# Optimization experiments

Measured on AMD Instinct MI355X. Metric: run time of the kernel, lower is better.

The kernel has to match this reference:

```python
import jax, jax.numpy as jnp
import numpy as np

D = 256; NH = 8; HD = D // NH; L = 4; P = 4; NQ = 900; BS = 8; DFFN = 1024
SHAPES = np.array([[128, 128], [64, 64], [32, 32], [16, 16]])  # (H, W) per level, static metadata
NV = int((SHAPES[:, 0] * SHAPES[:, 1]).sum())
EPS = 1e-6


def setup_inputs():
    key = jax.random.key(0)
    ks = iter(jax.random.split(key, 48))

    def nrm(shape, scale=0.02):
        return jax.random.normal(next(ks), shape, jnp.float32) * scale

    lsi = np.concatenate([[0], np.cumsum(SHAPES[:, 0] * SHAPES[:, 1])[:-1]]).astype(np.int64)
    return {
        'tgt': nrm((NQ, BS, D), 1.0),
        'tgt_query_pos': nrm((NQ, BS, D), 1.0),
        'tgt_reference_points': jax.random.uniform(next(ks), (NQ, BS, L, 2), jnp.float32),
        'memory': nrm((NV, BS, D), 1.0),
        'memory_spatial_shapes': jnp.asarray(SHAPES, jnp.int32),
        'memory_level_start_index': jnp.asarray(lsi, jnp.int32),
        'w_norm_sa': jnp.ones((D,), jnp.float32),
        'w_norm_ca': jnp.ones((D,), jnp.float32),
        'w_norm_ffn': jnp.ones((D,), jnp.float32),
        'ls_sa': jnp.full((D,), 1e-4, jnp.float32),
        'ls_ca': jnp.full((D,), 1e-4, jnp.float32),
        'ls_ffn': jnp.full((D,), 1e-4, jnp.float32),
        'Wq': nrm((D, D)), 'Wk': nrm((D, D)), 'Wv': nrm((D, D)),
        'bq': jnp.zeros((D,), jnp.float32), 'bk': jnp.zeros((D,), jnp.float32), 'bv': jnp.zeros((D,), jnp.float32),
        'Wo_sa': nrm((D, D)), 'bo_sa': jnp.zeros((D,), jnp.float32),
        'Wv_proj': nrm((D, D)), 'bv_proj': jnp.zeros((D,), jnp.float32),
        'W_off': nrm((NH * L * P * 2, D)), 'b_off': nrm((NH * L * P * 2,), 0.1),
        'W_attn': nrm((NH * L * P, D)), 'b_attn': jnp.zeros((NH * L * P,), jnp.float32),
        'W_out_ca': nrm((D, D)), 'bo_ca': jnp.zeros((D,), jnp.float32),
        'Wg': nrm((DFFN, D)), 'bg': jnp.zeros((DFFN,), jnp.float32),
        'Wu': nrm((DFFN, D)), 'bu': jnp.zeros((DFFN,), jnp.float32),
        'Wf': nrm((D, DFFN)), 'bf': jnp.zeros((D,), jnp.float32),
    }


def rmsnorm(x, w):
    return x * jax.lax.rsqrt(jnp.mean(x * x, axis=-1, keepdims=True) + EPS) * w


def ms_deform_sample(v, loc, attw):
    # v: (bs, nv, NH, HD); loc: (bs, nq, NH, L, P, 2) normalized (x, y); attw: (bs, nq, NH, L, P)
    bs, nq = loc.shape[0], loc.shape[1]
    out = jnp.zeros((bs, nq, NH, HD), loc.dtype)
    b_idx = jnp.arange(bs)[:, None, None, None]
    h_idx = jnp.arange(NH)[None, None, :, None]
    start = 0
    for l in range(L):
        Hl, Wl = int(SHAPES[l, 0]), int(SHAPES[l, 1])
        vf = v[:, start:start + Hl * Wl]  # (bs, Hl*Wl, NH, HD)
        start += Hl * Wl
        # grid_sample(align_corners=False, padding=zeros) pixel mapping
        x = loc[:, :, :, l, :, 0] * Wl - 0.5
        y = loc[:, :, :, l, :, 1] * Hl - 0.5
        x0 = jnp.floor(x)
        y0 = jnp.floor(y)
        acc = jnp.zeros((bs, nq, NH, P, HD), loc.dtype)
        for dx in (0, 1):
            for dy in (0, 1):
                xi = x0 + dx
                yi = y0 + dy
                w = (1.0 - jnp.abs(x - xi)) * (1.0 - jnp.abs(y - yi))
                valid = (xi >= 0) & (xi <= Wl - 1) & (yi >= 0) & (yi <= Hl - 1)
                w = jnp.where(valid, w, 0.0)
                idx = (jnp.clip(yi, 0, Hl - 1) * Wl + jnp.clip(xi, 0, Wl - 1)).astype(jnp.int32)
                acc = acc + w[..., None] * vf[b_idx, idx, h_idx]  # (bs, nq, NH, P, HD)
        out = out + jnp.einsum('bqhp,bqhpd->bqhd', attw[:, :, :, l], acc)
    return out


def reference(tgt, tgt_query_pos, tgt_reference_points, memory, memory_spatial_shapes,
              memory_level_start_index, w_norm_sa, w_norm_ca, w_norm_ffn, ls_sa, ls_ca, ls_ffn,
              Wq, Wk, Wv, bq, bk, bv, Wo_sa, bo_sa, Wv_proj, bv_proj, W_off, b_off, W_attn,
              b_attn, W_out_ca, bo_ca, Wg, bg, Wu, bu, Wf, bf):
    nq, bs, d = tgt.shape
    # --- self-attention (pre-norm + LayerScale residual) ---
    xn = rmsnorm(tgt, w_norm_sa)
    qk = xn + tgt_query_pos
    q = (qk @ Wq.T + bq).reshape(nq, bs, NH, HD)
    k = (qk @ Wk.T + bk).reshape(nq, bs, NH, HD)
    vv = (xn @ Wv.T + bv).reshape(nq, bs, NH, HD)
    scores = jnp.einsum('qbhd,kbhd->bhqk', q, k) * (1.0 / np.sqrt(HD))
    attn = jax.nn.softmax(scores, axis=-1)
    sa = jnp.einsum('bhqk,kbhd->qbhd', attn, vv).reshape(nq, bs, d) @ Wo_sa.T + bo_sa
    tgt = tgt + ls_sa * sa
    # --- multi-scale deformable cross-attention (identity=zeros in original) ---
    xn = rmsnorm(tgt, w_norm_ca)
    qca = jnp.swapaxes(xn + tgt_query_pos, 0, 1)  # (bs, nq, d)
    val = (jnp.swapaxes(memory, 0, 1) @ Wv_proj.T + bv_proj).reshape(bs, -1, NH, HD)
    off = (qca @ W_off.T + b_off).reshape(bs, nq, NH, L, P, 2)
    attw = jax.nn.softmax((qca @ W_attn.T + b_attn).reshape(bs, nq, NH, L * P), axis=-1)
    attw = attw.reshape(bs, nq, NH, L, P)
    norm = jnp.asarray(SHAPES[:, ::-1].copy(), jnp.float32)  # (W, H) per level
    ref = jnp.swapaxes(tgt_reference_points, 0, 1)  # (bs, nq, L, 2)
    loc = ref[:, :, None, :, None, :] + off / norm[None, None, None, :, None, :]
    ca = ms_deform_sample(val, loc, attw).reshape(bs, nq, d) @ W_out_ca.T + bo_ca
    tgt = tgt + ls_ca * jnp.swapaxes(ca, 0, 1)
    # --- SwiGLU FFN ---
    xn = rmsnorm(tgt, w_norm_ffn)
    ffn = (jax.nn.silu(xn @ Wg.T + bg) * (xn @ Wu.T + bu)) @ Wf.T + bf
    return tgt + ls_ffn * ffn
```

## Files before the change

### kernel.cpp

```cpp
#include <hip/hip_runtime.h>

typedef unsigned short ushort_t;
typedef unsigned int uint32;
typedef __bf16 bf16x8 __attribute__((ext_vector_type(8)));
typedef float f32x4 __attribute__((ext_vector_type(4)));
typedef ushort_t us4 __attribute__((ext_vector_type(4)));

#define D_    256
#define NH_   8
#define HD_   32
#define NQ_   900
#define BS_   8
#define TOK_  7200
#define NV_   21760
#define QP_   928
#define DFFN_ 1024

__device__ __forceinline__ ushort_t f2bf(float x) {
    union { float f; uint32 u; } v; v.f = x;
    uint32 r = v.u + 0x7FFFu + ((v.u >> 16) & 1u);
    return (ushort_t)(r >> 16);
}
__device__ __forceinline__ float bf2f(ushort_t h) {
    union { uint32 u; float f; } v; v.u = ((uint32)h) << 16;
    return v.f;
}
__device__ __forceinline__ int imin(int a, int b) { return a < b ? a : b; }
__device__ __forceinline__ int imax(int a, int b) { return a > b ? a : b; }

__global__ __launch_bounds__(256) void cvtall_k(
    const float* __restrict__ s0, const float* __restrict__ s1, const float* __restrict__ s2,
    const float* __restrict__ s3, const float* __restrict__ s4, const float* __restrict__ s5,
    const float* __restrict__ s6, const float* __restrict__ s7, const float* __restrict__ s8,
    const float* __restrict__ s9, const float* __restrict__ s10, ushort_t* __restrict__ dst,
    const float* __restrict__ bq, const float* __restrict__ bk,
    const float* __restrict__ boff, const float* __restrict__ battn,
    float* __restrict__ bias_qk, float* __restrict__ bias_ol) {
    int tid = threadIdx.x;
    if (blockIdx.x == 0) {
        bias_qk[tid] = bq[tid];
        bias_qk[256 + tid] = bk[tid];
        bias_ol[tid] = boff[tid];
        if (tid < 128) bias_ol[256 + tid] = battn[tid];
    }
    int id = blockIdx.x * 256 + tid;
    const float* s; int off;
    if      (id <  16384) { s = s0;  off = id; }
    else if (id <  32768) { s = s1;  off = id - 16384; }
    else if (id <  49152) { s = s2;  off = id - 32768; }
    else if (id <  65536) { s = s3;  off = id - 49152; }
    else if (id <  81920) { s = s4;  off = id - 65536; }
    else if (id <  98304) { s = s5;  off = id - 81920; }
    else if (id < 114688) { s = s6;  off = id - 98304; }
    else if (id < 122880) { s = s7;  off = id - 114688; }
    else if (id < 188416) { s = s8;  off = id - 122880; }
    else if (id < 253952) { s = s9;  off = id - 188416; }
    else                  { s = s10; off = id - 253952; }
    f32x4 v = *(const f32x4*)(s + (size_t)off * 4);
    us4 t;
#pragma unroll
    for (int e = 0; e < 4; e++) t[e] = f2bf(v[e]);
    *(us4*)(dst + (size_t)id * 4) = t;
}

__global__ __launch_bounds__(256) void rms_k(const float* __restrict__ x,
                                             const float* __restrict__ pos,
                                             const float* __restrict__ wn,
                                             ushort_t* __restrict__ xn_out,
                                             ushort_t* __restrict__ qk_out) {
    int r = blockIdx.x, tid = threadIdx.x;
    float v = x[r * D_ + tid];
    float ss = v * v;
#pragma unroll
    for (int o = 32; o; o >>= 1) ss += __shfl_xor(ss, o, 64);
    __shared__ float part[4];
    if ((tid & 63) == 0) part[tid >> 6] = ss;
    __syncthreads();
    float tot = part[0] + part[1] + part[2] + part[3];
    float sc = rsqrtf(tot * (1.f / 256.f) + 1e-6f);
    float xn = v * sc * wn[tid];
    if (xn_out) xn_out[r * D_ + tid] = f2bf(xn);
    if (qk_out) qk_out[r * D_ + tid] = f2bf(xn + pos[r * D_ + tid]);
}

enum { EPI_RESID, EPI_QK2, EPI_VT, EPI_VAL, EPI_OFFLOG };

template <int EPI, bool AF32, int BM, int BN, int WGM, int WGN, int TK>
__global__ __launch_bounds__(WGM * WGN * 64) void gemm2_k(
    const void* __restrict__ Ap, const ushort_t* __restrict__ Wp,
    const float* __restrict__ bias, void* __restrict__ outp, void* __restrict__ outp2,
    int M, int N, int swz,
    const float* __restrict__ resid, const float* __restrict__ ls, float scale) {
    constexpr int THREADS = WGM * WGN * 64;
    constexpr int NK  = TK / 32;
    constexpr int LDK = 40;
    constexpr int WR  = BM / WGM, WC = BN / WGN;
    constexpr int FM  = WR / 16,  FN = WC / 16;
    constexpr int ACH = AF32 ? (BM * 32 / 4 / THREADS) : (BM * 32 / 8 / THREADS);
    constexpr int BCH = BN * 32 / 8 / THREADS;

    __shared__ __align__(16) ushort_t As[2][BM * LDK];
    __shared__ __align__(16) ushort_t Bs[2][BN * LDK];

    const int tid = threadIdx.x, l = tid & 63, w = tid >> 6;
    const int wm = w % WGM, wn = w / WGM;
    int by = blockIdx.y;
    if (swz) { int cpx = gridDim.y >> 3; by = (by & 7) * cpx + (by >> 3); }
    const int m0 = by * BM, n0 = blockIdx.x * BN;
    const int lr = l & 15, lkb = (l >> 4) * 8;

    const ushort_t* Ab = (const ushort_t*)Ap;
    const float*    Af = (const float*)Ap;

    int aRow[ACH], aK[ACH], bRow[BCH], bK[BCH];
#pragma unroll
    for (int ch = 0; ch < ACH; ch++) {
        int cid = ch * THREADS + tid;
        if constexpr (AF32) { aRow[ch] = cid >> 3; aK[ch] = (cid & 7) * 4; }
        else                { aRow[ch] = cid >> 2; aK[ch] = (cid & 3) * 8; }
    }
#pragma unroll
    for (int ch = 0; ch < BCH; ch++) {
        int cid = ch * THREADS + tid;
        bRow[ch] = cid >> 2; bK[ch] = (cid & 3) * 8;
    }
    int aGRow[ACH];
#pragma unroll
    for (int ch = 0; ch < ACH; ch++) aGRow[ch] = imin(m0 + aRow[ch], M - 1);

    f32x4  aSTf[AF32 ? ACH : 1];
    bf16x8 aSTb[AF32 ? 1 : ACH];
    bf16x8 bST[BCH];

    auto load_regs = [&](int kt) {
        const int k0 = kt * 32;
#pragma unroll
        for (int ch = 0; ch < ACH; ch++) {
            if constexpr (AF32)
                aSTf[ch] = *(const f32x4*)(Af + (size_t)aGRow[ch] * TK + k0 + aK[ch]);
            else
                aSTb[ch] = *(const bf16x8*)(Ab + (size_t)aGRow[ch] * TK + k0 + aK[ch]);
        }
#pragma unroll
        for (int ch = 0; ch < BCH; ch++)
            bST[ch] = *(const bf16x8*)(Wp + (size_t)(n0 + bRow[ch]) * TK + k0 + bK[ch]);
    };
    auto write_lds = [&](int buf) {
#pragma unroll
        for (int ch = 0; ch < ACH; ch++) {
            if constexpr (AF32) {
                us4 t;
#pragma unroll
                for (int e = 0; e < 4; e++) t[e] = f2bf(aSTf[ch][e]);
                *(us4*)&As[buf][aRow[ch] * LDK + aK[ch]] = t;
            } else {
                *(bf16x8*)&As[buf][aRow[ch] * LDK + aK[ch]] = aSTb[ch];
            }
        }
#pragma unroll
        for (int ch = 0; ch < BCH; ch++)
            *(bf16x8*)&Bs[buf][bRow[ch] * LDK + bK[ch]] = bST[ch];
    };

    f32x4 acc[FM][FN];
#pragma unroll
    for (int i = 0; i < FM; i++)
#pragma unroll
        for (int j = 0; j < FN; j++) acc[i][j] = f32x4{0.f, 0.f, 0.f, 0.f};

    load_regs(0);
    write_lds(0);
    __syncthreads();

    for (int kt = 0; kt < NK; ++kt) {
        const int c = kt & 1;
        if (kt + 1 < NK) load_regs(kt + 1);

        bf16x8 af[FM], bf_[FN];
#pragma unroll
        for (int i = 0; i < FM; i++)
            af[i] = *(const bf16x8*)&As[c][(wm * WR + i * 16 + lr) * LDK + lkb];
#pragma unroll
        for (int j = 0; j < FN; j++)
            bf_[j] = *(const bf16x8*)&Bs[c][(wn * WC + j * 16 + lr) * LDK + lkb];
#pragma unroll
        for (int i = 0; i < FM; i++)
#pragma unroll
            for (int j = 0; j < FN; j++)
                acc[i][j] = __builtin_amdgcn_mfma_f32_16x16x32_bf16(af[i], bf_[j], acc[i][j], 0, 0, 0);

        if (kt + 1 < NK) write_lds(c ^ 1);
        __syncthreads();
    }

#pragma unroll
    for (int i = 0; i < FM; i++)
#pragma unroll
        for (int j = 0; j < FN; j++) {
            int col = n0 + wn * WC + j * 16 + lr;
            float bvv = bias[col];
#pragma unroll
            for (int e = 0; e < 4; e++) {
                int row = m0 + wm * WR + i * 16 + (l >> 4) * 4 + e;
                if (row >= M) continue;
                float v = acc[i][j][e] + bvv;
                if constexpr (EPI == EPI_RESID) {
                    size_t idx = (size_t)row * N + col;
                    ((float*)outp)[idx] = resid[idx] + ls[col] * v;
                } else if constexpr (EPI == EPI_QK2) {
                    int c2 = col & 255;
                    int q = row >> 3, bb = row & 7, h = c2 >> 5, hd = c2 & 31;
                    ushort_t* dst = (col < 256) ? (ushort_t*)outp : (ushort_t*)outp2;
                    float sc = (col < 256) ? scale : 1.f;
                    dst[((bb * NH_ + h) * QP_ + q) * HD_ + hd] = f2bf(v * sc);
                } else if constexpr (EPI == EPI_VT) {
                    int q = row >> 3, bb = row & 7, h = col >> 5, hd = col & 31;
                    ((ushort_t*)outp)[((bb * NH_ + h) * HD_ + hd) * QP_ + q] = f2bf(v);
                } else if constexpr (EPI == EPI_VAL) {
                    int vv = row >> 3, bb = row & 7, h = col >> 5, d = col & 31;
                    ((ushort_t*)outp)[(((size_t)(bb * NH_ + h)) * NV_ + vv) * HD_ + d] = f2bf(v);
                } else if constexpr (EPI == EPI_OFFLOG) {
                    if (col < 256) ((float*)outp)[(size_t)row * 256 + col] = v;
                    else           ((float*)outp2)[(size_t)row * 128 + col - 256] = v;
                }
            }
        }
}

__global__ __launch_bounds__(256) void ffn_k(
    const ushort_t* __restrict__ Ap, const ushort_t* __restrict__ Wg,
    const ushort_t* __restrict__ Wu, const float* __restrict__ bgp,
    const float* __restrict__ bup, ushort_t* __restrict__ outp, int M) {
    constexpr int BM = 64, BN = 128, TK = 256, NK = TK / 32, LDK = 40;
    constexpr int WR = 32, WC = 64, FM = 2, FN = 4;

    __shared__ __align__(16) ushort_t As[2][BM * LDK];
    __shared__ __align__(16) ushort_t Gs[2][BN * LDK];
    __shared__ __align__(16) ushort_t Us[2][BN * LDK];

    const int tid = threadIdx.x, l = tid & 63, w = tid >> 6;
    const int wm = w & 1, wn = w >> 1;
    const int m0 = blockIdx.y * BM, n0 = blockIdx.x * BN;
    const int lr = l & 15, lkb = (l >> 4) * 8;

    const int aRow = tid >> 2, aK = (tid & 3) * 8;
    int bRow[2], bK[2];
#pragma unroll
    for (int ch = 0; ch < 2; ch++) { int cid = ch * 256 + tid; bRow[ch] = cid >> 2; bK[ch] = (cid & 3) * 8; }
    const int aGRow = imin(m0 + aRow, M - 1);

    bf16x8 aST, gST[2], uST[2];
    auto load_regs = [&](int kt) {
        const int k0 = kt * 32;
        aST = *(const bf16x8*)(Ap + (size_t)aGRow * TK + k0 + aK);
#pragma unroll
        for (int ch = 0; ch < 2; ch++) {
            gST[ch] = *(const bf16x8*)(Wg + (size_t)(n0 + bRow[ch]) * TK + k0 + bK[ch]);
            uST[ch] = *(const bf16x8*)(Wu + (size_t)(n0 + bRow[ch]) * TK + k0 + bK[ch]);
        }
    };
    auto write_lds = [&](int buf) {
        *(bf16x8*)&As[buf][aRow * LDK + aK] = aST;
#pragma unroll
        for (int ch = 0; ch < 2; ch++) {
            *(bf16x8*)&Gs[buf][bRow[ch] * LDK + bK[ch]] = gST[ch];
            *(bf16x8*)&Us[buf][bRow[ch] * LDK + bK[ch]] = uST[ch];
        }
    };

    f32x4 accG[FM][FN], accU[FM][FN];
#pragma unroll
    for (int i = 0; i < FM; i++)
#pragma unroll
        for (int j = 0; j < FN; j++) { accG[i][j] = f32x4{0,0,0,0}; accU[i][j] = f32x4{0,0,0,0}; }

    load_regs(0);
    write_lds(0);
    __syncthreads();

    for (int kt = 0; kt < NK; ++kt) {
        const int c = kt & 1;
        if (kt + 1 < NK) load_regs(kt + 1);
        bf16x8 af[FM], gf[FN], uf[FN];
#pragma unroll
        for (int i = 0; i < FM; i++)
            af[i] = *(const bf16x8*)&As[c][(wm * WR + i * 16 + lr) * LDK + lkb];
#pragma unroll
        for (int j = 0; j < FN; j++) {
            gf[j] = *(const bf16x8*)&Gs[c][(wn * WC + j * 16 + lr) * LDK + lkb];
            uf[j] = *(const bf16x8*)&Us[c][(wn * WC + j * 16 + lr) * LDK + lkb];
        }
#pragma unroll
        for (int i = 0; i < FM; i++)
#pragma unroll
            for (int j = 0; j < FN; j++) {
                accG[i][j] = __builtin_amdgcn_mfma_f32_16x16x32_bf16(af[i], gf[j], accG[i][j], 0, 0, 0);
                accU[i][j] = __builtin_amdgcn_mfma_f32_16x16x32_bf16(af[i], uf[j], accU[i][j], 0, 0, 0);
            }
        if (kt + 1 < NK) write_lds(c ^ 1);
        __syncthreads();
    }

#pragma unroll
    for (int i = 0; i < FM; i++)
#pragma unroll
        for (int j = 0; j < FN; j++) {
            int col = n0 + wn * WC + j * 16 + lr;
            float bg_ = bgp[col], bu_ = bup[col];
#pragma unroll
            for (int e = 0; e < 4; e++) {
                int row = m0 + wm * WR + i * 16 + (l >> 4) * 4 + e;
                if (row >= M) continue;
                float g = accG[i][j][e] + bg_;
                float u = accU[i][j][e] + bu_;
                float s = g / (1.f + __expf(-g));
                outp[(size_t)row * DFFN_ + col] = f2bf(s * u);
            }
        }
}

__global__ __launch_bounds__(256) void attn2_k(const ushort_t* __restrict__ qb,
                                               const ushort_t* __restrict__ kb,
                                               const ushort_t* __restrict__ vtb,
                                               ushort_t* __restrict__ sab) {
    __shared__ __align__(16) ushort_t Pl[4][16 * 40];
    const int tid = threadIdx.x, l = tid & 63, w = tid >> 6;
    const int bh = blockIdx.y, b = bh >> 3, h = bh & 7;
    const int q0 = (blockIdx.x * 4 + w) * 16;
    if (q0 >= NQ_) return;
    const int q = l & 15, g = l >> 4;
    ushort_t* Pw = &Pl[w][0];

    const bf16x8 qf = *(const bf16x8*)(qb + ((size_t)bh * QP_ + q0 + q) * HD_ + g * 8);
    const ushort_t* kbase = kb + (size_t)bh * QP_ * HD_;
    const ushort_t* vbase = vtb + (size_t)bh * HD_ * QP_;

    f32x4 O0 = {0.f, 0.f, 0.f, 0.f}, O1 = {0.f, 0.f, 0.f, 0.f};
    float m = -1e30f, sl = 0.f;

    auto ldk = [&](int t, int u) {
        return *(const bf16x8*)(kbase + (size_t)(t * 32 + u * 16 + q) * HD_ + g * 8);
    };
    auto ldv = [&](int t, int dh) {
        return *(const bf16x8*)(vbase + (size_t)(dh * 16 + q) * QP_ + t * 32 + g * 8);
    };
    bf16x8 kA = ldk(0, 0), kB = ldk(0, 1), v0 = ldv(0, 0), v1 = ldv(0, 1);

    for (int t = 0; t < 29; ++t) {
        bf16x8 nkA, nkB, nv0, nv1;
        if (t < 28) { nkA = ldk(t + 1, 0); nkB = ldk(t + 1, 1); nv0 = ldv(t + 1, 0); nv1 = ldv(t + 1, 1); }
        const f32x4 z = {0.f, 0.f, 0.f, 0.f};
        f32x4 sA = __builtin_amdgcn_mfma_f32_16x16x32_bf16(kA, qf, z, 0, 0, 0);
        f32x4 sB = __builtin_amdgcn_mfma_f32_16x16x32_bf16(kB, qf, z, 0, 0, 0);
        if (t == 28) {
            int k0 = 896 + g * 4;
#pragma unroll
            for (int e = 0; e < 4; e++) {
                if (k0 + e >= NQ_)      sA[e] = -1e30f;
                if (k0 + 16 + e >= NQ_) sB[e] = -1e30f;
            }
        }
        float tm = fmaxf(fmaxf(fmaxf(sA[0], sA[1]), fmaxf(sA[2], sA[3])),
                         fmaxf(fmaxf(sB[0], sB[1]), fmaxf(sB[2], sB[3])));
        tm = fmaxf(tm, __shfl_xor(tm, 16, 64));
        tm = fmaxf(tm, __shfl_xor(tm, 32, 64));
        float mn = fmaxf(m, tm);
        float r = exp2f(m - mn);
        m = mn;
#pragma unroll
        for (int e = 0; e < 4; e++) { O0[e] *= r; O1[e] *= r; }
        float pA[4], pB[4], ps = 0.f;
#pragma unroll
        for (int e = 0; e < 4; e++) {
            pA[e] = exp2f(sA[e] - m); pB[e] = exp2f(sB[e] - m);
            ps += pA[e] + pB[e];
        }
        sl = sl * r + ps;
        uint32 a0, a1, b0, b1;
        asm("v_cvt_pk_bf16_f32 %0, %1, %2" : "=v"(a0) : "v"(pA[0]), "v"(pA[1]));
        asm("v_cvt_pk_bf16_f32 %0, %1, %2" : "=v"(a1) : "v"(pA[2]), "v"(pA[3]));
        asm("v_cvt_pk_bf16_f32 %0, %1, %2" : "=v"(b0) : "v"(pB[0]), "v"(pB[1]));
        asm("v_cvt_pk_bf16_f32 %0, %1, %2" : "=v"(b1) : "v"(pB[2]), "v"(pB[3]));
        { uint2 tt; tt.x = a0; tt.y = a1; *(uint2*)(Pw + q * 40 + g * 4) = tt; }
        { uint2 tt; tt.x = b0; tt.y = b1; *(uint2*)(Pw + q * 40 + 16 + g * 4) = tt; }
        bf16x8 pf = *(const bf16x8*)(Pw + q * 40 + g * 8);
        O0 = __builtin_amdgcn_mfma_f32_16x16x32_bf16(v0, pf, O0, 0, 0, 0);
        O1 = __builtin_amdgcn_mfma_f32_16x16x32_bf16(v1, pf, O1, 0, 0, 0);
        kA = nkA; kB = nkB; v0 = nv0; v1 = nv1;
    }

    sl += __shfl_xor(sl, 16, 64);
    sl += __shfl_xor(sl, 32, 64);
    float inv = 1.f / sl;
    int row_q = q0 + q;
    if (row_q < NQ_) {
        ushort_t* op = sab + ((size_t)row_q * BS_ + b) * D_ + h * HD_ + g * 4;
#pragma unroll
        for (int dh = 0; dh < 2; dh++) {
            f32x4 Ov = dh ? O1 : O0;
            float e0 = Ov[0] * inv, e1 = Ov[1] * inv, e2 = Ov[2] * inv, e3 = Ov[3] * inv;
            uint32 w0, w1;
            asm("v_cvt_pk_bf16_f32 %0, %1, %2" : "=v"(w0) : "v"(e0), "v"(e1));
            asm("v_cvt_pk_bf16_f32 %0, %1, %2" : "=v"(w1) : "v"(e2), "v"(e3));
            *(uint32*)(op + dh * 16) = w0;
            *(uint32*)(op + dh * 16 + 2) = w1;
        }
    }
}

__global__ __launch_bounds__(256) void deform_k(
    const float* __restrict__ offb, const float* __restrict__ logb,
    const float* __restrict__ refpts, const int* __restrict__ shapes,
    const int* __restrict__ lsi, const ushort_t* __restrict__ val,
    ushort_t* __restrict__ ca) {
    __shared__ float off_l[256];
    __shared__ float attw[128];
    const int r = blockIdx.x;
    const int b = r & 7;
    const int tid = threadIdx.x;

    off_l[tid] = offb[(size_t)r * 256 + tid];
    if (tid < 128) {
        float lg = logb[(size_t)r * 128 + tid];
        float m = lg;
#pragma unroll
        for (int o = 1; o < 16; o <<= 1) m = fmaxf(m, __shfl_xor(m, o, 16));
        float e = __expf(lg - m);
        float s = e;
#pragma unroll
        for (int o = 1; o < 16; o <<= 1) s += __shfl_xor(s, o, 16);
        attw[tid] = e / s;
    }
    __syncthreads();

    const int h = tid >> 5, d = tid & 31;
    const ushort_t* vb = val + ((size_t)(b * NH_ + h)) * NV_ * HD_;
    float acc = 0.f;
#pragma unroll
    for (int lvl = 0; lvl < 4; lvl++) {
        const int H = shapes[lvl * 2], W = shapes[lvl * 2 + 1];
        const int base = lsi[lvl];
        const float refx = refpts[(r * 4 + lvl) * 2];
        const float refy = refpts[(r * 4 + lvl) * 2 + 1];
#pragma unroll
        for (int p = 0; p < 4; p++) {
            int oi = ((h * 4 + lvl) * 4 + p) * 2;
            float x = (refx + off_l[oi] / (float)W) * (float)W - 0.5f;
            float y = (refy + off_l[oi + 1] / (float)H) * (float)H - 0.5f;
            float x0 = floorf(x), y0 = floorf(y);
            float fx = x - x0, fy = y - y0;
            int ix = (int)x0, iy = (int)y0;
            float sval = 0.f;
#pragma unroll
            for (int dy = 0; dy <= 1; dy++)
#pragma unroll
                for (int dx = 0; dx <= 1; dx++) {
                    int xi = ix + dx, yi = iy + dy;
                    float wq = (dx ? fx : 1.f - fx) * (dy ? fy : 1.f - fy);
                    if (xi < 0 || xi >= W || yi < 0 || yi >= H) wq = 0.f;
                    int cx = imin(imax(xi, 0), W - 1), cy = imin(imax(yi, 0), H - 1);
                    float vv = bf2f(vb[(size_t)(base + cy * W + cx) * HD_ + d]);
                    sval += wq * vv;
                }
            acc += attw[h * 16 + lvl * 4 + p] * sval;
        }
    }
    ca[(size_t)r * 256 + tid] = f2bf(acc);
}

extern "C" void kernel_launch(void* const* d_in, const int* in_sizes, int n_in,
                              void* d_out, int out_size, void* d_ws, size_t ws_size,
                              hipStream_t stream) {
    (void)in_sizes; (void)n_in; (void)out_size; (void)ws_size;
    const float* tgt    = (const float*)d_in[0];
    const float* qpos   = (const float*)d_in[1];
    const float* refp   = (const float*)d_in[2];
    const float* mem    = (const float*)d_in[3];
    const int*   shapes = (const int*)d_in[4];
    const int*   lsi    = (const int*)d_in[5];
    const float* wnsa   = (const float*)d_in[6];
    const float* wnca   = (const float*)d_in[7];
    const float* wnffn  = (const float*)d_in[8];
    const float* lssa   = (const float*)d_in[9];
    const float* lsca   = (const float*)d_in[10];
    const float* lsffn  = (const float*)d_in[11];
    const float* Wq = (const float*)d_in[12];
    const float* Wk = (const float*)d_in[13];
    const float* Wv = (const float*)d_in[14];
    const float* bq = (const float*)d_in[15];
    const float* bk = (const float*)d_in[16];
    const float* bvv = (const float*)d_in[17];
    const float* Wo_sa = (const float*)d_in[18];
    const float* bo_sa = (const float*)d_in[19];
    const float* Wv_proj = (const float*)d_in[20];
    const float* bv_proj = (const float*)d_in[21];
    const float* W_off = (const float*)d_in[22];
    const float* b_off = (const float*)d_in[23];
    const float* W_attn = (const float*)d_in[24];
    const float* b_attn = (const float*)d_in[25];
    const float* W_out = (const float*)d_in[26];
    const float* bo_ca = (const float*)d_in[27];
    const float* Wg = (const float*)d_in[28];
    const float* bg = (const float*)d_in[29];
    const float* Wu = (const float*)d_in[30];
    const float* bu = (const float*)d_in[31];
    const float* Wf = (const float*)d_in[32];
    const float* bff = (const float*)d_in[33];

    char* ws = (char*)d_ws;
    size_t o = 0;
    auto alloc = [&](size_t b) { size_t c = o; o += (b + 255) & ~(size_t)255; return c; };

    const size_t wq_o = alloc(65536 * 2), wk_o = alloc(65536 * 2), wv_o = alloc(65536 * 2);
    const size_t wosa_o = alloc(65536 * 2), wvp_o = alloc(65536 * 2), wout_o = alloc(65536 * 2);
    const size_t woff_o = alloc(65536 * 2), wattn_o = alloc(32768 * 2);
    const size_t wg_o = alloc(262144 * 2), wu_o = alloc(262144 * 2), wf_o = alloc(262144 * 2);
    const size_t bqk_o = alloc(512 * 4), bol_o = alloc(384 * 4);
    const size_t xnsa_o = alloc((size_t)TOK_ * D_ * 2);
    const size_t qksa_o = alloc((size_t)TOK_ * D_ * 2);
    const size_t qkvBytes = (size_t)BS_ * NH_ * QP_ * HD_ * 2;
    const size_t qb_o = alloc(qkvBytes);
    const size_t kb_o = alloc(qkvBytes);
    const size_t vt_o = alloc(qkvBytes + 512);
    const size_t sa_o = alloc((size_t)TOK_ * D_ * 2);
    const size_t tgt1_o = alloc((size_t)TOK_ * D_ * 4);
    const size_t qca_o = alloc((size_t)TOK_ * D_ * 2);
    const size_t offb_o = alloc((size_t)TOK_ * 256 * 4);
    const size_t logit_o = alloc((size_t)TOK_ * 128 * 4);
    const size_t ca_o = alloc((size_t)TOK_ * D_ * 2);
    const size_t tgt2_o = alloc((size_t)TOK_ * D_ * 4);
    const size_t val_o = alloc((size_t)NV_ * BS_ * D_ * 2);
    const size_t h_o  = val_o;
    const size_t xn3_o = h_o + (size_t)TOK_ * DFFN_ * 2;

    dim3 blk(256);
    cvtall_k<<<dim3(319488 / 256), blk, 0, stream>>>(
        Wq, Wk, Wv, Wo_sa, Wv_proj, W_out, W_off, W_attn, Wg, Wu, Wf,
        (ushort_t*)(ws + wq_o),
        bq, bk, b_off, b_attn, (float*)(ws + bqk_o), (float*)(ws + bol_o));

    (void)hipMemsetAsync(ws + vt_o, 0, qkvBytes + 512, stream);

    rms_k<<<dim3(TOK_), blk, 0, stream>>>(tgt, qpos, wnsa,
                                          (ushort_t*)(ws + xnsa_o), (ushort_t*)(ws + qksa_o));
    const float QSC = 0.25503321550239915f;
    gemm2_k<EPI_QK2, false, 64, 128, 2, 2, 256><<<dim3(4, 113), blk, 0, stream>>>(
        ws + qksa_o, (ushort_t*)(ws + wq_o), (const float*)(ws + bqk_o),
        ws + qb_o, ws + kb_o, TOK_, 512, 0, nullptr, nullptr, QSC);
    gemm2_k<EPI_VT, false, 64, 128, 2, 2, 256><<<dim3(2, 113), blk, 0, stream>>>(
        ws + xnsa_o, (ushort_t*)(ws + wv_o), bvv, ws + vt_o, nullptr, TOK_, 256, 0,
        nullptr, nullptr, 1.f);
    attn2_k<<<dim3(15, 64), blk, 0, stream>>>((ushort_t*)(ws + qb_o), (ushort_t*)(ws + kb_o),
                                              (ushort_t*)(ws + vt_o), (ushort_t*)(ws + sa_o));
    gemm2_k<EPI_RESID, false, 64, 128, 2, 2, 256><<<dim3(2, 113), blk, 0, stream>>>(
        ws + sa_o, (ushort_t*)(ws + wosa_o), bo_sa, ws + tgt1_o, nullptr, TOK_, 256, 0,
        tgt, lssa, 1.f);

    rms_k<<<dim3(TOK_), blk, 0, stream>>>((const float*)(ws + tgt1_o), qpos, wnca,
                                          nullptr, (ushort_t*)(ws + qca_o));
    gemm2_k<EPI_OFFLOG, false, 64, 128, 2, 2, 256><<<dim3(3, 113), blk, 0, stream>>>(
        ws + qca_o, (ushort_t*)(ws + woff_o), (const float*)(ws + bol_o),
        ws + offb_o, ws + logit_o, TOK_, 384, 0, nullptr, nullptr, 1.f);
    gemm2_k<EPI_VAL, true, 128, 256, 2, 4, 256><<<dim3(1, 1360), dim3(512), 0, stream>>>(
        mem, (ushort_t*)(ws + wvp_o), bv_proj, ws + val_o, nullptr, NV_ * BS_, 256, 1,
        nullptr, nullptr, 1.f);
    deform_k<<<dim3(TOK_), blk, 0, stream>>>(
        (const float*)(ws + offb_o), (const float*)(ws + logit_o), refp, shapes, lsi,
        (ushort_t*)(ws + val_o), (ushort_t*)(ws + ca_o));
    gemm2_k<EPI_RESID, false, 64, 128, 2, 2, 256><<<dim3(2, 113), blk, 0, stream>>>(
        ws + ca_o, (ushort_t*)(ws + wout_o), bo_ca, ws + tgt2_o, nullptr, TOK_, 256, 0,
        (const float*)(ws + tgt1_o), lsca, 1.f);

    rms_k<<<dim3(TOK_), blk, 0, stream>>>((const float*)(ws + tgt2_o), nullptr, wnffn,
                                          (ushort_t*)(ws + xn3_o), nullptr);
    ffn_k<<<dim3(8, 113), blk, 0, stream>>>(
        (const ushort_t*)(ws + xn3_o), (const ushort_t*)(ws + wg_o),
        (const ushort_t*)(ws + wu_o), bg, bu, (ushort_t*)(ws + h_o), TOK_);
    gemm2_k<EPI_RESID, false, 64, 128, 2, 2, 1024><<<dim3(2, 113), blk, 0, stream>>>(
        ws + h_o, (ushort_t*)(ws + wf_o), bff, d_out, nullptr, TOK_, 256, 0,
        (const float*)(ws + tgt2_o), lsffn, 1.f);
}
```

Measured before the change: 340.4 us.

## Add dedicated value-projection GEMM streaming fp32 A from registers with resident weight tile

Replaces the generic templated GEMM for the memory value projection with a specialized kernel. Each block keeps its whole 128x256 bf16 weight slice in shared memory and streams fp32 rows of memory straight from global into registers, prefetching the next K step and converting to bf16 before the MFMA. The grid changes from 1x1360 blocks with 128x256 tiles to 2x1360 blocks with 128x128 tiles. This removes the shared-memory staging of A and its syncs, and splitting N in two means each A row is read from global twice. The row swizzle of blocks is kept.

Result: slower. 388.6 us (+14.2%).

```diff
diff --git a/kernel.cpp b/kernel.cpp
--- a/kernel.cpp
+++ b/kernel.cpp
@@ -223,6 +223,92 @@
                     if (col < 256) ((float*)outp)[(size_t)row * 256 + col] = v;
                     else           ((float*)outp2)[(size_t)row * 128 + col - 256] = v;
                 }
+            }
+        }
+}
+
+__global__ __launch_bounds__(512, 4) void gemm3_k(
+    const float* __restrict__ Af, const ushort_t* __restrict__ Wp,
+    const float* __restrict__ bias, ushort_t* __restrict__ outp, int swz) {
+    constexpr int TK = 256, NK = 8, LDK = 264;
+    __shared__ __align__(16) ushort_t Bs[128 * LDK];
+
+    const int tid = threadIdx.x, l = tid & 63, w = tid >> 6;
+    const int wm = w & 3, wn = w >> 2;
+    int by = blockIdx.y;
+    if (swz) { int cpx = gridDim.y >> 3; by = (by & 7) * cpx + (by >> 3); }
+    const int m0 = by * 128, n0 = blockIdx.x * 128;
+    const int lr = l & 15, g = l >> 4, lkb = g * 8;
+
+    {
+        const int r2 = tid >> 5, c2 = (tid & 31) * 8;
+#pragma unroll
+        for (int ch = 0; ch < 8; ch++) {
+            bf16x8 t = *(const bf16x8*)(Wp + (size_t)(n0 + r2 + ch * 16) * TK + c2);
+            *(bf16x8*)&Bs[(r2 + ch * 16) * LDK + c2] = t;
+        }
+    }
+    __syncthreads();
+
+    const int arow = m0 + wm * 32 + lr;
+    const float* aBase = Af + (size_t)arow * TK + lkb;
+
+    f32x4 aC[2][2];
+#pragma unroll
+    for (int i = 0; i < 2; i++) {
+        const f32x4* p = (const f32x4*)(aBase + (size_t)i * 16 * TK);
+        aC[i][0] = p[0]; aC[i][1] = p[1];
+    }
+
+    f32x4 acc[2][4];
+#pragma unroll
+    for (int i = 0; i < 2; i++)
+#pragma unroll
+        for (int j = 0; j < 4; j++) acc[i][j] = f32x4{0.f, 0.f, 0.f, 0.f};
+
+    for (int kt = 0; kt < NK; ++kt) {
+        f32x4 aN[2][2];
+        if (kt + 1 < NK) {
+#pragma unroll
+            for (int i = 0; i < 2; i++) {
+                const f32x4* p = (const f32x4*)(aBase + (size_t)i * 16 * TK + (kt + 1) * 32);
+                aN[i][0] = p[0]; aN[i][1] = p[1];
+            }
+        }
+        bf16x8 af[2];
+#pragma unroll
+        for (int i = 0; i < 2; i++)
+#pragma unroll
+            for (int e = 0; e < 4; e++) {
+                af[i][e]     = (__bf16)aC[i][0][e];
+                af[i][4 + e] = (__bf16)aC[i][1][e];
+            }
+        bf16x8 bfr[4];
+#pragma unroll
+        for (int j = 0; j < 4; j++)
+            bfr[j] = *(const bf16x8*)&Bs[(wn * 64 + j * 16 + lr) * LDK + kt * 32 + lkb];
+#pragma unroll
+        for (int i = 0; i < 2; i++)
+#pragma unroll
+            for (int j = 0; j < 4; j++)
+                acc[i][j] = __builtin_amdgcn_mfma_f32_16x16x32_bf16(af[i], bfr[j], acc[i][j], 0, 0, 0);
+#pragma unroll
+        for (int i = 0; i < 2; i++) { aC[i][0] = aN[i][0]; aC[i][1] = aN[i][1]; }
+    }
+
+#pragma unroll
+    for (int i = 0; i < 2; i++)
+#pragma unroll
+        for (int j = 0; j < 4; j++) {
+            int col = n0 + wn * 64 + j * 16 + lr;
+            float bvv = bias[col];
+            int h = col >> 5, d = col & 31;
+#pragma unroll
+            for (int e = 0; e < 4; e++) {
+                int row = m0 + wm * 32 + i * 16 + g * 4 + e;
+                int vv = row >> 3, bb = row & 7;
+                float v = acc[i][j][e] + bvv;
+                outp[(((size_t)(bb * NH_ + h)) * NV_ + vv) * HD_ + d] = f2bf(v);
             }
         }
 }
@@ -561,9 +647,8 @@
     gemm2_k<EPI_OFFLOG, false, 64, 128, 2, 2, 256><<<dim3(3, 113), blk, 0, stream>>>(
         ws + qca_o, (ushort_t*)(ws + woff_o), (const float*)(ws + bol_o),
         ws + offb_o, ws + logit_o, TOK_, 384, 0, nullptr, nullptr, 1.f);
-    gemm2_k<EPI_VAL, true, 128, 256, 2, 4, 256><<<dim3(1, 1360), dim3(512), 0, stream>>>(
-        mem, (ushort_t*)(ws + wvp_o), bv_proj, ws + val_o, nullptr, NV_ * BS_, 256, 1,
-        nullptr, nullptr, 1.f);
+    gemm3_k<<<dim3(2, 1360), dim3(512), 0, stream>>>(
+        mem, (ushort_t*)(ws + wvp_o), bv_proj, (ushort_t*)(ws + val_o), 1);
     deform_k<<<dim3(TOK_), blk, 0, stream>>>(
         (const float*)(ws + offb_o), (const float*)(ws + logit_o), refp, shapes, lsi,
         (ushort_t*)(ws + val_o), (ushort_t*)(ws + ca_o));
```

## Deepen GEMM global-load prefetch to two K-tiles with dual register staging

Applied to the files above, without the earlier changes.

Restructures the GEMM main loop to keep two register staging sets, so global loads for tile k+2 and k+3 are issued while tile k is computed, with the loop unrolled by two over the LDS double buffer. The aim is to hide more global memory latency behind the MFMA work. It roughly doubles staging register use, which can lower occupancy, and it assumes NK is even (true for K=256/1024 with 32-wide tiles); if NK were odd, wrl1 would read a tile that was never loaded.

Measured after the change: 352.2 us. +3.5%, slower.

```diff
diff --git a/kernel.cpp b/kernel.cpp
--- a/kernel.cpp
+++ b/kernel.cpp
@@ -128,38 +128,67 @@
 #pragma unroll
     for (int ch = 0; ch < ACH; ch++) aGRow[ch] = imin(m0 + aRow[ch], M - 1);
 
-    f32x4  aSTf[AF32 ? ACH : 1];
-    bf16x8 aSTb[AF32 ? 1 : ACH];
-    bf16x8 bST[BCH];
-
-    auto load_regs = [&](int kt) {
+    f32x4  aSTf0[AF32 ? ACH : 1], aSTf1[AF32 ? ACH : 1];
+    bf16x8 aSTb0[AF32 ? 1 : ACH], aSTb1[AF32 ? 1 : ACH];
+    bf16x8 bST0[BCH], bST1[BCH];
+
+    auto load0 = [&](int kt) {
         const int k0 = kt * 32;
 #pragma unroll
         for (int ch = 0; ch < ACH; ch++) {
             if constexpr (AF32)
-                aSTf[ch] = *(const f32x4*)(Af + (size_t)aGRow[ch] * TK + k0 + aK[ch]);
+                aSTf0[ch] = *(const f32x4*)(Af + (size_t)aGRow[ch] * TK + k0 + aK[ch]);
             else
-                aSTb[ch] = *(const bf16x8*)(Ab + (size_t)aGRow[ch] * TK + k0 + aK[ch]);
+                aSTb0[ch] = *(const bf16x8*)(Ab + (size_t)aGRow[ch] * TK + k0 + aK[ch]);
         }
 #pragma unroll
         for (int ch = 0; ch < BCH; ch++)
-            bST[ch] = *(const bf16x8*)(Wp + (size_t)(n0 + bRow[ch]) * TK + k0 + bK[ch]);
-    };
-    auto write_lds = [&](int buf) {
+            bST0[ch] = *(const bf16x8*)(Wp + (size_t)(n0 + bRow[ch]) * TK + k0 + bK[ch]);
+    };
+    auto load1 = [&](int kt) {
+        const int k0 = kt * 32;
+#pragma unroll
+        for (int ch = 0; ch < ACH; ch++) {
+            if constexpr (AF32)
+                aSTf1[ch] = *(const f32x4*)(Af + (size_t)aGRow[ch] * TK + k0 + aK[ch]);
+            else
+                aSTb1[ch] = *(const bf16x8*)(Ab + (size_t)aGRow[ch] * TK + k0 + aK[ch]);
+        }
+#pragma unroll
+        for (int ch = 0; ch < BCH; ch++)
+            bST1[ch] = *(const bf16x8*)(Wp + (size_t)(n0 + bRow[ch]) * TK + k0 + bK[ch]);
+    };
+    auto wrl0 = [&](int buf) {
 #pragma unroll
         for (int ch = 0; ch < ACH; ch++) {
             if constexpr (AF32) {
                 us4 t;
 #pragma unroll
-                for (int e = 0; e < 4; e++) t[e] = f2bf(aSTf[ch][e]);
+                for (int e = 0; e < 4; e++) t[e] = f2bf(aSTf0[ch][e]);
                 *(us4*)&As[buf][aRow[ch] * LDK + aK[ch]] = t;
             } else {
-                *(bf16x8*)&As[buf][aRow[ch] * LDK + aK[ch]] = aSTb[ch];
+                *(bf16x8*)&As[buf][aRow[ch] * LDK + aK[ch]] = aSTb0[ch];
             }
         }
 #pragma unroll
         for (int ch = 0; ch < BCH; ch++)
-            *(bf16x8*)&Bs[buf][bRow[ch] * LDK + bK[ch]] = bST[ch];
+            *(bf16x8*)&Bs[buf][bRow[ch] * LDK + bK[ch]] = bST0[ch];
+    };
+    auto wrl1 = [&](int buf) {
+#pragma unroll
+        for (int ch = 0; ch < ACH; ch++) {
+            if constexpr (AF32) {
+                us4 t;
+#pragma unroll
+                for (int e = 0; e < 4; e++) t[e] = f2bf(aSTf1[ch][e]);
+                *(us4*)&As[buf][aRow[ch] * LDK + aK[ch]] = t;
+            } else {
+                *(bf16x8*)&As[buf][aRow[ch] * LDK + aK[ch]] = aSTb1[ch];
+            }
+        }
+#pragma unroll
+        for (int ch = 0; ch < BCH; ch++)
+            *(bf16x8*)&Bs[buf][bRow[ch] * LDK + bK[ch]] = bST1[ch];
     };
 
     f32x4 acc[FM][FN];
@@ -168,14 +197,7 @@
 #pragma unroll
         for (int j = 0; j < FN; j++) acc[i][j] = f32x4{0.f, 0.f, 0.f, 0.f};
 
-    load_regs(0);
-    write_lds(0);
-    __syncthreads();
-
-    for (int kt = 0; kt < NK; ++kt) {
-        const int c = kt & 1;
-        if (kt + 1 < NK) load_regs(kt + 1);
-
+    auto compute = [&](int c) {
         bf16x8 af[FM], bf_[FN];
 #pragma unroll
         for (int i = 0; i < FM; i++)
@@ -188,8 +210,21 @@
 #pragma unroll
             for (int j = 0; j < FN; j++)
                 acc[i][j] = __builtin_amdgcn_mfma_f32_16x16x32_bf16(af[i], bf_[j], acc[i][j], 0, 0, 0);
-
-        if (kt + 1 < NK) write_lds(c ^ 1);
+    };
+
+    load0(0);
+    load1(1);
+    wrl0(0);
+    __syncthreads();
+
+    for (int kt = 0; kt < NK; kt += 2) {
+        if (kt + 2 < NK) load0(kt + 2);
+        compute(0);
+        wrl1(1);
+        __syncthreads();
+        if (kt + 3 < NK) load1(kt + 3);
+        compute(1);
+        if (kt + 2 < NK) wrl0(0);
         __syncthreads();
     }
 
```
